# Optimization experiments

Hardware: AMD Instinct MI355X
Metric: run time of the kernel (lower is better)

The kernel has to match this reference:

```python
import jax, jax.numpy as jnp
import numpy as np

EPS = 1e-5
K = 27  # 3x3x3 kernel taps


def conv3d(x, w, b):
    # x: [B,C,D,H,W], w: [O,I,3,3,3], SAME padding == pad 1, stride 1
    out = jax.lax.conv_general_dilated(
        x, w, window_strides=(1, 1, 1), padding='SAME',
        dimension_numbers=('NCDHW', 'OIDHW', 'NCDHW'))
    return out + b.reshape(1, -1, 1, 1, 1)


def batchnorm(x, gamma, beta):
    # training-mode BN over (B,D,H,W), matching nn.BatchNorm3d in train()
    m = x.mean(axis=(0, 2, 3, 4), keepdims=True)
    v = x.var(axis=(0, 2, 3, 4), keepdims=True)
    return (x - m) * jax.lax.rsqrt(v + EPS) * gamma.reshape(1, -1, 1, 1, 1) + beta.reshape(1, -1, 1, 1, 1)


def trilinear_gather(xg, pd, ph, pw):
    # xg: [cpg,D,H,W]; pd/ph/pw: [K,D,H,W] float sample positions.
    # Zero-padding outside the volume (invalid corners contribute 0).
    D, H, W = xg.shape[1], xg.shape[2], xg.shape[3]
    d0, h0, w0 = jnp.floor(pd), jnp.floor(ph), jnp.floor(pw)
    fd, fh, fw = pd - d0, ph - h0, pw - w0
    out = jnp.zeros((xg.shape[0],) + pd.shape, xg.dtype)
    for dd in (0, 1):
        for hh in (0, 1):
            for ww in (0, 1):
                d_, h_, w_ = d0 + dd, h0 + hh, w0 + ww
                wt = ((fd if dd else 1.0 - fd)
                      * (fh if hh else 1.0 - fh)
                      * (fw if ww else 1.0 - fw))
                valid = ((d_ >= 0) & (d_ < D) & (h_ >= 0) & (h_ < H)
                         & (w_ >= 0) & (w_ < W))
                di = jnp.clip(d_, 0, D - 1).astype(jnp.int32)
                hi = jnp.clip(h_, 0, H - 1).astype(jnp.int32)
                wi = jnp.clip(w_, 0, W - 1).astype(jnp.int32)
                vals = xg[:, di, hi, wi]  # [cpg,K,D,H,W]
                out = out + vals * (wt * valid)[None]
    return out


def deform_conv3d(x, off, w, G, cpg):
    # x: [B,C,D,H,W]; off: [B,G*K*3,D,H,W]; w: [O,C,3,3,3]
    B, C, D, H, W = x.shape
    k = jnp.arange(K)
    kd = (k // 9 - 1).astype(x.dtype)
    kh = (k // 3 % 3 - 1).astype(x.dtype)
    kw = (k % 3 - 1).astype(x.dtype)
    off = off.reshape(B, G, K, 3, D, H, W)
    pd = off[:, :, :, 0] + kd[:, None, None, None] + jnp.arange(D, dtype=x.dtype)[:, None, None]
    ph = off[:, :, :, 1] + kh[:, None, None, None] + jnp.arange(H, dtype=x.dtype)[:, None]
    pw = off[:, :, :, 2] + kw[:, None, None, None] + jnp.arange(W, dtype=x.dtype)
    xg = x.reshape(B, G, cpg, D, H, W)
    gather = jax.vmap(jax.vmap(trilinear_gather))  # over B, then G
    cols = gather(xg, pd, ph, pw)  # [B,G,cpg,K,D,H,W]
    wg = w.reshape(w.shape[0], G, cpg, K)
    return jnp.einsum('bgckdhw,ogck->bodhw', cols, wg)


def setup_inputs() -> dict:
    key = jax.random.key(0)
    B, C, D, H, W = 2, 64, 8, 56, 56
    cpg = 8
    G = C // cpg
    OFFC = G * 3 * K  # 648
    ks = jax.random.split(key, 12)
    inp = {
        'x': jax.random.normal(ks[0], (B, C, D, H, W), jnp.float32),
        'w_off1': jax.random.normal(ks[1], (OFFC, C, 3, 3, 3), jnp.float32) * 0.01,
        'b_off1': jax.random.normal(ks[2], (OFFC,), jnp.float32) * 0.01,
        'w_dc1': jax.random.normal(ks[3], (C, C, 3, 3, 3), jnp.float32) * 0.05,
        'gamma1': jnp.ones((C,), jnp.float32),
        'beta1': jnp.zeros((C,), jnp.float32),
        'w_off2': jax.random.normal(ks[4], (OFFC, C, 3, 3, 3), jnp.float32) * 0.01,
        'b_off2': jax.random.normal(ks[5], (OFFC,), jnp.float32) * 0.01,
        'w_dc2': jax.random.normal(ks[6], (C, C, 3, 3, 3), jnp.float32) * 0.05,
        'gamma2': jnp.ones((C,), jnp.float32),
        'beta2': jnp.zeros((C,), jnp.float32),
    }
    return inp


def reference(x, w_off1, b_off1, w_dc1, gamma1, beta1,
              w_off2, b_off2, w_dc2, gamma2, beta2):
    cpg = 8
    G = x.shape[1] // cpg
    residual = x
    off = conv3d(x, w_off1, b_off1)
    h = deform_conv3d(x, off, w_dc1, G, cpg)
    h = jax.nn.relu(batchnorm(h, gamma1, beta1))
    off = conv3d(h, w_off2, b_off2)
    h = deform_conv3d(h, off, w_dc2, G, cpg)
    h = batchnorm(h, gamma2, beta2)
    return jax.nn.relu(h + residual)
```

## Files before the change

kernel.cpp:

```cpp
#include <hip/hip_runtime.h>

#define B_    2
#define C_    64
#define D_    8
#define H_    56
#define W_    56
#define HW_   3136
#define DHW_  25088
#define G_    8
#define K_    27
#define OFFC_ 648

#define PD_   10
#define PH_   58
#define PW_   58
#define PSPAT (PD_ * PH_ * PW_)
#define PGSZ  (PSPAT * 8)

#define PACKB ((B_ * G_ * PSPAT + 255) / 256)
#define TG1   ((OFFC_ * 2048) / 256)
#define TG2   ((C_ * 1728) / 256)

typedef __attribute__((ext_vector_type(8))) short  bf16x8;
typedef __attribute__((ext_vector_type(4))) float  f32x4;
typedef __attribute__((ext_vector_type(8))) unsigned short ushort8;

__device__ __forceinline__ unsigned short f2bf(float f) {
    unsigned u = __float_as_uint(f);
    u = (u + 0x7FFFu + ((u >> 16) & 1u)) >> 16;
    return (unsigned short)u;
}
__device__ __forceinline__ float bf2f(unsigned short u) {
    return __uint_as_float(((unsigned)u) << 16);
}
__device__ __forceinline__ unsigned cvt_pk_bf16(float lo, float hi) {
    unsigned r;
    asm("v_cvt_pk_bf16_f32 %0, %1, %2" : "=v"(r) : "v"(lo), "v"(hi));
    return r;
}
__device__ __forceinline__ void gload_lds16(const void* g, void* l) {
    __builtin_amdgcn_global_load_lds(
        (const __attribute__((address_space(1))) unsigned int*)g,
        (__attribute__((address_space(3))) unsigned int*)l, 16, 0, 0);
}

__global__ __launch_bounds__(256) void prep_kernel(
    const float* __restrict__ x, unsigned short* __restrict__ xp, int npack,
    const float* __restrict__ woff, unsigned short* __restrict__ wT2,
    const float* __restrict__ wdc, unsigned short* __restrict__ wdcT)
{
    int blk = blockIdx.x;
    const int t = threadIdx.x;
    if (blk < npack) {
        int i = blk * 256 + t;
        if (i >= B_ * G_ * PSPAT) return;
        int b = i / (G_ * PSPAT);
        int rem = i - b * G_ * PSPAT;
        int g = rem / PSPAT, s = rem - g * PSPAT;
        int dp = s / (PH_ * PW_), r2 = s - dp * (PH_ * PW_);
        int hp = r2 / PW_, wp = r2 - hp * PW_;
        ushort8 v = {0, 0, 0, 0, 0, 0, 0, 0};
        if (dp >= 1 && dp <= D_ && hp >= 1 && hp <= H_ && wp >= 1 && wp <= W_) {
            const float* src = x + (size_t)(b * C_ + g * 8) * DHW_ + (dp - 1) * HW_ + (hp - 1) * W_ + (wp - 1);
            #pragma unroll
            for (int c = 0; c < 8; ++c) v[c] = f2bf(src[c * DHW_]);
        }
        *(ushort8*)(xp + (size_t)i * 8) = v;
        return;
    }
    blk -= npack;
    if (blk < TG1) {
        int i = blk * 256 + t;
        int oc = i >> 11, r = i & 2047;
        int g = r >> 8, r2 = r & 255;
        int s = r2 >> 3, c = r2 & 7;
        int tap = s ^ (oc & 7);
        unsigned short v = 0;
        if (tap < 27) v = f2bf(woff[(size_t)oc * 1728 + (g * 8 + c) * 27 + tap]);
        wT2[i] = v;
        return;
    }
    blk -= TG1;
    {
        int i = blk * 256 + t;
        int oc = i / 1728, k = i - oc * 1728;
        int icc = k / 216, r = k - icc * 216;
        int tap = r >> 3, icl = r & 7;
        wdcT[i] = f2bf(wdc[(size_t)oc * 1728 + (icc * 8 + icl) * 27 + tap]);
    }
}

#define CROW 512
__device__ __forceinline__ int swz(int row, int kByte) {
    return row * CROW + (kByte ^ ((row & 7) << 4));
}

#define XRH 12
__global__ __launch_bounds__(256, 2) void conv_off_mfma_kernel(
    const unsigned short* __restrict__ xpad, const unsigned short* __restrict__ wT2,
    const float* __restrict__ bias, unsigned short* __restrict__ out)
{
    __shared__ __align__(16) char wb[64 * CROW];
    __shared__ __align__(16) unsigned short xr[3 * XRH * 64 * 8];

    const int oc0  = blockIdx.x * 64;
    const int pos0 = blockIdx.y * 512;
    const int b    = blockIdx.z >> 3;
    const int d    = blockIdx.z & 7;
    const int h0   = pos0 / 56;
    const int t    = threadIdx.x;
    const int lane = t & 63;
    const int li   = lane & 15;
    const int ts   = lane >> 4;
    const int wv   = t >> 6;

    int poff[8];
    #pragma unroll
    for (int pb = 0; pb < 8; ++pb) {
        int p  = pos0 + wv * 128 + pb * 16 + li;
        int pc = p < HW_ ? p : HW_ - 1;
        int hp = pc / 56, wp = pc - hp * 56;
        poff[pb] = (hp - h0) * 64 + wp;
    }
    int offk[7];
    #pragma unroll
    for (int kk = 0; kk < 7; ++kk) {
        int tap = min(4 * kk + ts, 26);
        int dd = tap / 9, hh = (tap / 3) % 3, ww = tap - (tap / 3) * 3;
        offk[kk] = (dd * XRH + hh) * 64 + ww;
    }

    int xsrc[9];
    #pragma unroll
    for (int it = 0; it < 9; ++it) {
        int i = it * 256 + t;
        int w = i & 63, rest = i >> 6;
        int hl = rest % XRH, dd = rest / XRH;
        int dp = d + dd;
        int hp = min(h0 + hl, PH_ - 1);
        int wp = min(w, PW_ - 1);
        xsrc[it] = ((dp * PH_ + hp) * PW_ + wp) * 8;
    }
    size_t wsrc[8];
    #pragma unroll
    for (int it = 0; it < 8; ++it) {
        int j = it * 256 + t;
        int rowg = min(oc0 + (j >> 5), OFFC_ - 1);
        wsrc[it] = ((size_t)rowg * 8) * 256 + (size_t)(j & 31) * 8;
    }

    f32x4 acc[4][8];
    #pragma unroll
    for (int i = 0; i < 4; ++i)
        #pragma unroll
        for (int j = 0; j < 8; ++j) acc[i][j] = (f32x4){0.f, 0.f, 0.f, 0.f};

    const unsigned short* xb0 = xpad + (size_t)(b * 8) * PGSZ;

    for (int g = 0; g < 8; ++g) {
        __syncthreads();
        const unsigned short* xb = xb0 + (size_t)g * PGSZ;
        #pragma unroll
        for (int it = 0; it < 9; ++it)
            gload_lds16(xb + xsrc[it], &xr[(it * 256 + t) * 8]);
        const unsigned short* wg = wT2 + (size_t)g * 256;
        #pragma unroll
        for (int it = 0; it < 8; ++it)
            gload_lds16(wg + wsrc[it], wb + (size_t)(it * 256 + t) * 16);
        __syncthreads();

        #pragma unroll
        for (int kk = 0; kk < 7; ++kk) {
            int tap = 4 * kk + ts;
            bf16x8 a[4];
            #pragma unroll
            for (int oa = 0; oa < 4; ++oa)
                a[oa] = *(const bf16x8*)(wb + swz(oa * 16 + li, tap * 16));
            #pragma unroll
            for (int pb = 0; pb < 8; ++pb) {
                bf16x8 bfrag = *(const bf16x8*)&xr[(offk[kk] + poff[pb]) * 8];
                #pragma unroll
                for (int oa = 0; oa < 4; ++oa)
                    acc[oa][pb] = __builtin_amdgcn_mfma_f32_16x16x32_bf16(a[oa], bfrag, acc[oa][pb], 0, 0, 0);
            }
        }
    }

    #pragma unroll
    for (int oa = 0; oa < 4; ++oa)
        #pragma unroll
        for (int pb = 0; pb < 8; ++pb)
            #pragma unroll
            for (int r = 0; r < 4; ++r) {
                int ocg = oc0 + oa * 16 + ts * 4 + r;
                int p   = pos0 + wv * 128 + pb * 16 + li;
                if (ocg < OFFC_ && p < HW_)
                    out[((size_t)(b * OFFC_ + ocg) * 8 + d) * HW_ + p] = f2bf(acc[oa][pb][r] + bias[ocg]);
            }
}

#define REDS 17
__global__ __launch_bounds__(256, 4) void deform_mfma_kernel(
    const unsigned short* __restrict__ xpad, const unsigned short* __restrict__ off,
    const unsigned short* __restrict__ wT, float* __restrict__ out)
{
    __shared__ float red[3 * 64 * REDS];

    const int id  = blockIdx.y * 196 + blockIdx.x;
    const int sid = (id & 7) * 392 + (id >> 3);
    const int pt  = sid % 196;
    const int bd  = sid / 196;
    const int b   = bd >> 3;
    const int d   = bd & 7;
    const int pos0 = pt * 16;

    const int t    = threadIdx.x;
    const int lane = t & 63;
    const int li   = lane & 15, ts = lane >> 4;
    const int wv   = t >> 6;

    const int p  = pos0 + li;
    const int hq = p / 56, wq = p - hq * 56;

    f32x4 acc[4];
    #pragma unroll
    for (int i = 0; i < 4; ++i) acc[i] = (f32x4){0.f, 0.f, 0.f, 0.f};

    #pragma unroll
    for (int gg = 0; gg < 2; ++gg) {
        const int g = wv * 2 + gg;
        const unsigned short* xg = xpad + (size_t)(b * 8 + g) * PGSZ;
        const unsigned short* wg = wT + g * 216;
        #pragma unroll
        for (int kk = 0; kk < 7; ++kk) {
            int tap = 4 * kk + ts;
            int tc  = tap < 27 ? tap : 26;
            bf16x8 afr[4];
            #pragma unroll
            for (int oa = 0; oa < 4; ++oa)
                afr[oa] = *(const bf16x8*)(wg + (size_t)(oa * 16 + li) * 1728 + tc * 8);
            bf16x8 bfr;
            {
                float a8[8] = {0.f, 0.f, 0.f, 0.f, 0.f, 0.f, 0.f, 0.f};
                if (tap < 27) {
                    int kd = tap / 9 - 1, kh = (tap / 3) % 3 - 1, kw = tap - (tap / 3) * 3 - 1;
                    size_t ob = ((size_t)(b * OFFC_ + (g * 27 + tap) * 3) * 8 + d) * HW_ + p;
                    float pd = bf2f(off[ob])            + (float)(kd + d);
                    float ph = bf2f(off[ob + DHW_])     + (float)(kh + hq);
                    float pw = bf2f(off[ob + 2 * DHW_]) + (float)(kw + wq);
                    float fd0 = floorf(pd), fh0 = floorf(ph), fw0 = floorf(pw);
                    float fd = pd - fd0, fh = ph - fh0, fw = pw - fw0;
                    int d0 = (int)fd0, h0i = (int)fh0, w0i = (int)fw0;
                    #pragma unroll
                    for (int tp = 0; tp < 8; ++tp) {
                        int dd = tp >> 2, hh = (tp >> 1) & 1, ww = tp & 1;
                        int di = d0 + dd, hi = h0i + hh, wi = w0i + ww;
                        float wgt = (dd ? fd : 1.f - fd) * (hh ? fh : 1.f - fh) * (ww ? fw : 1.f - fw);
                        bool valid = ((unsigned)di < 8u) && ((unsigned)hi < 56u) && ((unsigned)wi < 56u);
                        wgt = valid ? wgt : 0.f;
                        int dc = valid ? di : 0, hc = valid ? hi : 0, wc = valid ? wi : 0;
                        ushort8 v = *(const ushort8*)(xg + (((size_t)(dc + 1) * PH_ + hc + 1) * PW_ + wc + 1) * 8);
                        #pragma unroll
                        for (int c = 0; c < 8; ++c) a8[c] += bf2f(v[c]) * wgt;
                    }
                }
                union { unsigned u[4]; bf16x8 v; } cv;
                #pragma unroll
                for (int c = 0; c < 4; ++c) cv.u[c] = cvt_pk_bf16(a8[2 * c], a8[2 * c + 1]);
                bfr = cv.v;
            }
            #pragma unroll
            for (int oa = 0; oa < 4; ++oa)
                acc[oa] = __builtin_amdgcn_mfma_f32_16x16x32_bf16(afr[oa], bfr, acc[oa], 0, 0, 0);
        }
    }

    if (wv > 0) {
        float* rr = red + (wv - 1) * 64 * REDS + lane * REDS;
        #pragma unroll
        for (int oa = 0; oa < 4; ++oa)
            #pragma unroll
            for (int q = 0; q < 4; ++q)
                rr[oa * 4 + q] = acc[oa][q];
    }
    __syncthreads();
    if (wv == 0) {
        #pragma unroll
        for (int w2 = 0; w2 < 3; ++w2) {
            const float* rr = red + w2 * 64 * REDS + lane * REDS;
            #pragma unroll
            for (int oa = 0; oa < 4; ++oa)
                #pragma unroll
                for (int q = 0; q < 4; ++q)
                    acc[oa][q] += rr[oa * 4 + q];
        }
        #pragma unroll
        for (int oa = 0; oa < 4; ++oa)
            #pragma unroll
            for (int r = 0; r < 4; ++r) {
                int oc = oa * 16 + ts * 4 + r;
                out[((size_t)(b * C_ + oc) * 8 + d) * HW_ + p] = acc[oa][r];
            }
    }
}

__global__ __launch_bounds__(256) void bn_stats_partial_kernel(
    const float* __restrict__ h, float* __restrict__ part)
{
    const int c = blockIdx.x, s = blockIdx.y;
    const int t = threadIdx.x;
    const int SL = (B_ * DHW_) / 16;
    float sum = 0.f, sq = 0.f;
    for (int j = s * SL + t * 4; j < (s + 1) * SL; j += 1024) {
        int b = j / DHW_, i = j - b * DHW_;
        f32x4 v = *(const f32x4*)(h + (size_t)(b * C_ + c) * DHW_ + i);
        #pragma unroll
        for (int q = 0; q < 4; ++q) { sum += v[q]; sq += v[q] * v[q]; }
    }
    #pragma unroll
    for (int o = 32; o > 0; o >>= 1) {
        sum += __shfl_down(sum, o);
        sq  += __shfl_down(sq, o);
    }
    __shared__ float rs[4], rq[4];
    if ((t & 63) == 0) { rs[t >> 6] = sum; rq[t >> 6] = sq; }
    __syncthreads();
    if (t == 0) {
        part[c * 16 + s]        = rs[0] + rs[1] + rs[2] + rs[3];
        part[1024 + c * 16 + s] = rq[0] + rq[1] + rq[2] + rq[3];
    }
}

__global__ void bn_stats_finalize_kernel(
    const float* __restrict__ part, float* __restrict__ stats)
{
    int c = threadIdx.x;
    if (c >= 64) return;
    float s = 0.f, q = 0.f;
    for (int i = 0; i < 16; ++i) { s += part[c * 16 + i]; q += part[1024 + c * 16 + i]; }
    float inv = 1.f / (float)(B_ * DHW_);
    float m   = s * inv;
    float var = q * inv - m * m;
    stats[c]      = m;
    stats[C_ + c] = rsqrtf(fmaxf(var, 0.f) + 1e-5f);
}

__global__ __launch_bounds__(256) void bn_relu_pack_kernel(
    const float* __restrict__ h, const float* __restrict__ stats,
    const float* __restrict__ gamma, const float* __restrict__ beta,
    unsigned short* __restrict__ out)
{
    int i = blockIdx.x * 256 + threadIdx.x;
    if (i >= B_ * G_ * PSPAT) return;
    int b = i / (G_ * PSPAT);
    int rem = i - b * G_ * PSPAT;
    int g = rem / PSPAT, s = rem - g * PSPAT;
    int dp = s / (PH_ * PW_), r2 = s - dp * (PH_ * PW_);
    int hp = r2 / PW_, wp = r2 - hp * PW_;
    ushort8 o8 = {0, 0, 0, 0, 0, 0, 0, 0};
    if (dp >= 1 && dp <= D_ && hp >= 1 && hp <= H_ && wp >= 1 && wp <= W_) {
        int dhw = (dp - 1) * HW_ + (hp - 1) * W_ + (wp - 1);
        #pragma unroll
        for (int c = 0; c < 8; ++c) {
            int ch = g * 8 + c;
            float v = (h[(size_t)(b * C_ + ch) * DHW_ + dhw] - stats[ch]) * stats[C_ + ch] * gamma[ch] + beta[ch];
            o8[c] = f2bf(v > 0.f ? v : 0.f);
        }
    }
    *(ushort8*)(out + (size_t)i * 8) = o8;
}

__global__ __launch_bounds__(256) void bn_add_relu_kernel(
    float* __restrict__ hbuf, const float* __restrict__ xres,
    const float* __restrict__ stats,
    const float* __restrict__ gamma, const float* __restrict__ beta)
{
    const int n = B_ * C_ * DHW_;
    for (int i = blockIdx.x * 256 + threadIdx.x; i < n; i += gridDim.x * 256) {
        int c = (i / DHW_) & (C_ - 1);
        float v = (hbuf[i] - stats[c]) * stats[C_ + c] * gamma[c] + beta[c] + xres[i];
        hbuf[i] = v > 0.f ? v : 0.f;
    }
}

extern "C" void kernel_launch(void* const* d_in, const int* in_sizes, int n_in,
                              void* d_out, int out_size, void* d_ws, size_t ws_size,
                              hipStream_t stream)
{
    const float* x      = (const float*)d_in[0];
    const float* w_off1 = (const float*)d_in[1];
    const float* b_off1 = (const float*)d_in[2];
    const float* w_dc1  = (const float*)d_in[3];
    const float* gamma1 = (const float*)d_in[4];
    const float* beta1  = (const float*)d_in[5];
    const float* w_off2 = (const float*)d_in[6];
    const float* b_off2 = (const float*)d_in[7];
    const float* w_dc2  = (const float*)d_in[8];
    const float* gamma2 = (const float*)d_in[9];
    const float* beta2  = (const float*)d_in[10];
    float* out = (float*)d_out;

    unsigned short* offb = (unsigned short*)d_ws;
    unsigned short* xpad = offb + (size_t)B_ * OFFC_ * DHW_;
    unsigned short* h1pd = xpad + (size_t)B_ * G_ * PGSZ;
    unsigned short* wT2  = h1pd + (size_t)B_ * G_ * PGSZ;
    unsigned short* wdcT = wT2  + (size_t)OFFC_ * 2048;
    float* h1raw = (float*)(wdcT + (size_t)C_ * 1728);
    float* stats = h1raw + (size_t)B_ * C_ * DHW_;
    float* part  = stats + 128;

    dim3 cgrid(11, 7, B_ * D_);
    dim3 dgrid(196, B_ * D_);
    dim3 sgrid(C_, 16);

    prep_kernel             <<<PACKB + TG1 + TG2, 256, 0, stream>>>(x, xpad, PACKB, w_off1, wT2, w_dc1, wdcT);
    conv_off_mfma_kernel    <<<cgrid, 256, 0, stream>>>(xpad, wT2, b_off1, offb);
    deform_mfma_kernel      <<<dgrid, 256, 0, stream>>>(xpad, offb, wdcT, h1raw);
    bn_stats_partial_kernel <<<sgrid, 256, 0, stream>>>(h1raw, part);
    bn_stats_finalize_kernel<<<1, 64, 0, stream>>>(part, stats);
    bn_relu_pack_kernel     <<<PACKB, 256, 0, stream>>>(h1raw, stats, gamma1, beta1, h1pd);

    prep_kernel             <<<TG1 + TG2, 256, 0, stream>>>(nullptr, nullptr, 0, w_off2, wT2, w_dc2, wdcT);
    conv_off_mfma_kernel    <<<cgrid, 256, 0, stream>>>(h1pd, wT2, b_off2, offb);
    deform_mfma_kernel      <<<dgrid, 256, 0, stream>>>(h1pd, offb, wdcT, out);
    bn_stats_partial_kernel <<<sgrid, 256, 0, stream>>>(out, part);
    bn_stats_finalize_kernel<<<1, 64, 0, stream>>>(part, stats);
    bn_add_relu_kernel      <<<1024, 256, 0, stream>>>(out, x, stats, gamma2, beta2);
}
```

Measured before the change: 675.1 us.

## Split deform conv groups across two blocks and sum partials downstream

The deform conv kernel previously had each of its 4 waves handle 2 groups serially. It now launches twice as many blocks, each covering 4 groups with one group per wave. The two half-sums go to separate buffers (the output and a new hpart workspace), and the BN stats, BN-relu-pack and final BN-add-relu kernels add them when they read. This raises parallelism and shortens each block's serial work, at the cost of an extra full-size fp32 buffer write plus extra reads in three downstream kernels.

```diff
diff --git a/kernel.cpp b/kernel.cpp
--- a/kernel.cpp
+++ b/kernel.cpp
@@ -202,22 +202,26 @@
 #define REDS 17
 __global__ __launch_bounds__(256, 4) void deform_mfma_kernel(
     const unsigned short* __restrict__ xpad, const unsigned short* __restrict__ off,
-    const unsigned short* __restrict__ wT, float* __restrict__ out)
+    const unsigned short* __restrict__ wT, float* __restrict__ hout,
+    float* __restrict__ hpart)
 {
     __shared__ float red[3 * 64 * REDS];
 
-    const int id  = blockIdx.y * 196 + blockIdx.x;
-    const int sid = (id & 7) * 392 + (id >> 3);
-    const int pt  = sid % 196;
-    const int bd  = sid / 196;
-    const int b   = bd >> 3;
-    const int d   = bd & 7;
+    const int id   = blockIdx.y * 196 + blockIdx.x;
+    const int sid  = (id & 7) * 784 + (id >> 3);
+    const int pt   = sid % 196;
+    const int rest = sid / 196;
+    const int bd   = rest >> 1;
+    const int gs   = rest & 1;
+    const int b    = bd >> 3;
+    const int d    = bd & 7;
     const int pos0 = pt * 16;
 
     const int t    = threadIdx.x;
     const int lane = t & 63;
     const int li   = lane & 15, ts = lane >> 4;
     const int wv   = t >> 6;
+    const int g    = gs * 4 + wv;
 
     const int p  = pos0 + li;
     const int hq = p / 56, wq = p - hq * 56;
@@ -226,9 +230,7 @@
     #pragma unroll
     for (int i = 0; i < 4; ++i) acc[i] = (f32x4){0.f, 0.f, 0.f, 0.f};
 
-    #pragma unroll
-    for (int gg = 0; gg < 2; ++gg) {
-        const int g = wv * 2 + gg;
+    {
         const unsigned short* xg = xpad + (size_t)(b * 8 + g) * PGSZ;
         const unsigned short* wg = wT + g * 216;
         #pragma unroll
@@ -294,18 +296,19 @@
                 for (int q = 0; q < 4; ++q)
                     acc[oa][q] += rr[oa * 4 + q];
         }
+        float* dst = gs ? hpart : hout;
         #pragma unroll
         for (int oa = 0; oa < 4; ++oa)
             #pragma unroll
             for (int r = 0; r < 4; ++r) {
                 int oc = oa * 16 + ts * 4 + r;
-                out[((size_t)(b * C_ + oc) * 8 + d) * HW_ + p] = acc[oa][r];
+                dst[((size_t)(b * C_ + oc) * 8 + d) * HW_ + p] = acc[oa][r];
             }
     }
 }
 
 __global__ __launch_bounds__(256) void bn_stats_partial_kernel(
-    const float* __restrict__ h, float* __restrict__ part)
+    const float* __restrict__ ha, const float* __restrict__ hb, float* __restrict__ part)
 {
     const int c = blockIdx.x, s = blockIdx.y;
     const int t = threadIdx.x;
@@ -313,9 +316,11 @@
     float sum = 0.f, sq = 0.f;
     for (int j = s * SL + t * 4; j < (s + 1) * SL; j += 1024) {
         int b = j / DHW_, i = j - b * DHW_;
-        f32x4 v = *(const f32x4*)(h + (size_t)(b * C_ + c) * DHW_ + i);
-        #pragma unroll
-        for (int q = 0; q < 4; ++q) { sum += v[q]; sq += v[q] * v[q]; }
+        size_t base = (size_t)(b * C_ + c) * DHW_ + i;
+        f32x4 va = *(const f32x4*)(ha + base);
+        f32x4 vb = *(const f32x4*)(hb + base);
+        #pragma unroll
+        for (int q = 0; q < 4; ++q) { float v = va[q] + vb[q]; sum += v; sq += v * v; }
     }
     #pragma unroll
     for (int o = 32; o > 0; o >>= 1) {
@@ -346,7 +351,8 @@
 }
 
 __global__ __launch_bounds__(256) void bn_relu_pack_kernel(
-    const float* __restrict__ h, const float* __restrict__ stats,
+    const float* __restrict__ ha, const float* __restrict__ hb,
+    const float* __restrict__ stats,
     const float* __restrict__ gamma, const float* __restrict__ beta,
     unsigned short* __restrict__ out)
 {
@@ -363,7 +369,8 @@
         #pragma unroll
         for (int c = 0; c < 8; ++c) {
             int ch = g * 8 + c;
-            float v = (h[(size_t)(b * C_ + ch) * DHW_ + dhw] - stats[ch]) * stats[C_ + ch] * gamma[ch] + beta[ch];
+            size_t base = (size_t)(b * C_ + ch) * DHW_ + dhw;
+            float v = (ha[base] + hb[base] - stats[ch]) * stats[C_ + ch] * gamma[ch] + beta[ch];
             o8[c] = f2bf(v > 0.f ? v : 0.f);
         }
     }
@@ -371,14 +378,14 @@
 }
 
 __global__ __launch_bounds__(256) void bn_add_relu_kernel(
-    float* __restrict__ hbuf, const float* __restrict__ xres,
-    const float* __restrict__ stats,
+    float* __restrict__ hbuf, const float* __restrict__ hpart,
+    const float* __restrict__ xres, const float* __restrict__ stats,
     const float* __restrict__ gamma, const float* __restrict__ beta)
 {
     const int n = B_ * C_ * DHW_;
     for (int i = blockIdx.x * 256 + threadIdx.x; i < n; i += gridDim.x * 256) {
         int c = (i / DHW_) & (C_ - 1);
-        float v = (hbuf[i] - stats[c]) * stats[C_ + c] * gamma[c] + beta[c] + xres[i];
+        float v = (hbuf[i] + hpart[i] - stats[c]) * stats[C_ + c] * gamma[c] + beta[c] + xres[i];
         hbuf[i] = v > 0.f ? v : 0.f;
     }
 }
@@ -406,24 +413,25 @@
     unsigned short* wT2  = h1pd + (size_t)B_ * G_ * PGSZ;
     unsigned short* wdcT = wT2  + (size_t)OFFC_ * 2048;
     float* h1raw = (float*)(wdcT + (size_t)C_ * 1728);
-    float* stats = h1raw + (size_t)B_ * C_ * DHW_;
+    float* hpart = h1raw + (size_t)B_ * C_ * DHW_;
+    float* stats = hpart + (size_t)B_ * C_ * DHW_;
     float* part  = stats + 128;
 
     dim3 cgrid(11, 7, B_ * D_);
-    dim3 dgrid(196, B_ * D_);
+    dim3 dgrid(196, 32);
     dim3 sgrid(C_, 16);
 
     prep_kernel             <<<PACKB + TG1 + TG2, 256, 0, stream>>>(x, xpad, PACKB, w_off1, wT2, w_dc1, wdcT);
     conv_off_mfma_kernel    <<<cgrid, 256, 0, stream>>>(xpad, wT2, b_off1, offb);
-    deform_mfma_kernel      <<<dgrid, 256, 0, stream>>>(xpad, offb, wdcT, h1raw);
-    bn_stats_partial_kernel <<<sgrid, 256, 0, stream>>>(h1raw, part);
+    deform_mfma_kernel      <<<dgrid, 256, 0, stream>>>(xpad, offb, wdcT, h1raw, hpart);
+    bn_stats_partial_kernel <<<sgrid, 256, 0, stream>>>(h1raw, hpart, part);
     bn_stats_finalize_kernel<<<1, 64, 0, stream>>>(part, stats);
-    bn_relu_pack_kernel     <<<PACKB, 256, 0, stream>>>(h1raw, stats, gamma1, beta1, h1pd);
+    bn_relu_pack_kernel     <<<PACKB, 256, 0, stream>>>(h1raw, hpart, stats, gamma1, beta1, h1pd);
 
     prep_kernel             <<<TG1 + TG2, 256, 0, stream>>>(nullptr, nullptr, 0, w_off2, wT2, w_dc2, wdcT);
     conv_off_mfma_kernel    <<<cgrid, 256, 0, stream>>>(h1pd, wT2, b_off2, offb);
-    deform_mfma_kernel      <<<dgrid, 256, 0, stream>>>(h1pd, offb, wdcT, out);
-    bn_stats_partial_kernel <<<sgrid, 256, 0, stream>>>(out, part);
+    deform_mfma_kernel      <<<dgrid, 256, 0, stream>>>(h1pd, offb, wdcT, out, hpart);
+    bn_stats_partial_kernel <<<sgrid, 256, 0, stream>>>(out, hpart, part);
     bn_stats_finalize_kernel<<<1, 64, 0, stream>>>(part, stats);
-    bn_add_relu_kernel      <<<1024, 256, 0, stream>>>(out, x, stats, gamma2, beta2);
-}
+    bn_add_relu_kernel      <<<1024, 256, 0, stream>>>(out, hpart, x, stats, gamma2, beta2);
+}
```

Measured after the change: 660.9 us. 1.02x faster.
